# Kernel tuning notes

Hardware: AMD Instinct MI355X
Metric: run time of the kernel (lower is better)

## Reference

```python
import jax, jax.numpy as jnp
import numpy as np

# Module dims (match init_kwargs)
D_IN = 1024
N_PRI = 2048
D_PRI = 16
N_CLS = 25
D_CLS = 16
ITERS = 3
B = 64
EPS = 1e-6


def layer_norm(x, g, b, eps=1e-5):
    m = x.mean(-1, keepdims=True)
    v = ((x - m) ** 2).mean(-1, keepdims=True)
    return (x - m) / jnp.sqrt(v + eps) * g + b


def setup_inputs() -> dict:
    key = jax.random.key(0)
    ks = jax.random.split(key, 6)
    s = lambda n: 1.0 / np.sqrt(n)
    return {
        "z": jax.random.normal(ks[0], (B, D_IN), jnp.float32),
        # to_primary: Linear(d_in, n_primary*d_primary)
        "w1": jax.random.normal(ks[1], (D_IN, N_PRI * D_PRI), jnp.float32) * s(D_IN),
        "b1": jnp.zeros((N_PRI * D_PRI,), jnp.float32),
        # primary_act: LayerNorm(d_in) -> Linear(d_in, n_primary) -> Sigmoid
        "ln1_g": jnp.ones((D_IN,), jnp.float32),
        "ln1_b": jnp.zeros((D_IN,), jnp.float32),
        "w2": jax.random.normal(ks[2], (D_IN, N_PRI), jnp.float32) * s(D_IN),
        "b2": jnp.zeros((N_PRI,), jnp.float32),
        # CapsuleFC transform + EM routing params
        "w_caps": jax.random.normal(ks[3], (N_PRI, D_PRI, N_CLS, D_CLS), jnp.float32) * s(D_PRI),
        "beta_u": jnp.zeros((N_CLS,), jnp.float32),
        "beta_a": jnp.zeros((N_CLS,), jnp.float32),
        # to_logits: LayerNorm(d_class) -> Linear(d_class, 1)
        "ln2_g": jnp.ones((D_CLS,), jnp.float32),
        "ln2_b": jnp.zeros((D_CLS,), jnp.float32),
        "w3": jax.random.normal(ks[4], (D_CLS, 1), jnp.float32) * s(D_CLS),
        "b3": jnp.zeros((1,), jnp.float32),
    }


def em_routing(V, a_in, beta_u, beta_a, n_iter):
    # V: (b, n_in, n_out, d) votes; a_in: (b, n_in) primary activations
    b, n, o, d = V.shape
    R = jnp.full((b, n, o), 1.0 / o, V.dtype)  # routing assignments
    lam = jnp.asarray(1.0, V.dtype)            # inverse temperature
    for _ in range(n_iter):
        # M-step: weighted mean/variance per output capsule
        r = R * a_in[:, :, None]                                  # (b,n,o)
        r_sum = r.sum(axis=1) + EPS                               # (b,o)
        mu = jnp.einsum('bno,bnod->bod', r, V) / r_sum[..., None]  # (b,o,d)
        diff2 = (V - mu[:, None]) ** 2                            # (b,n,o,d)
        sigma2 = jnp.einsum('bno,bnod->bod', r, diff2) / r_sum[..., None] + EPS
        cost = (beta_u[None, :, None] + 0.5 * jnp.log(sigma2)) * r_sum[..., None]
        a_out = jax.nn.sigmoid(lam * (beta_a[None, :] - cost.sum(-1)))  # (b,o)
        # E-step: Gaussian log-likelihood of each vote under each output capsule
        logp = (-0.5 * (diff2 / sigma2[:, None]).sum(-1)
                - 0.5 * jnp.log(sigma2).sum(-1)[:, None, :])      # (b,n,o)
        R = jax.nn.softmax(jnp.log(a_out + EPS)[:, None, :] + logp, axis=-1)
    return mu, a_out, R


def reference(z, w1, b1, ln1_g, ln1_b, w2, b2, w_caps, beta_u, beta_a,
              ln2_g, ln2_b, w3, b3):
    b = z.shape[0]
    # primary poses (no squash: use_squash_primary=False)
    primary_pose = (z @ w1 + b1).reshape(b, N_PRI, D_PRI)
    # primary activations
    primary_act = jnp.clip(jax.nn.sigmoid(layer_norm(z, ln1_g, ln1_b) @ w2 + b2), 0.0, 1.0)
    # votes: each primary capsule predicts each class capsule's pose
    V = jnp.einsum('bni,niod->bnod', primary_pose, w_caps)  # (B, N_PRI, N_CLS, D_CLS)
    class_pose, class_act, q = em_routing(V, primary_act, beta_u, beta_a, ITERS)
    logits = (layer_norm(class_pose, ln2_g, ln2_b) @ w3 + b3).squeeze(-1)  # (B, N_CLS)
    acts = jnp.linalg.norm(class_pose, axis=-1)                            # (B, N_CLS)
    return logits, acts, class_pose, q
```

## Files before the change

### kernel.cpp

```cpp
#include <hip/hip_runtime.h>
#include <hip/hip_bf16.h>
#include <cstdio>

#define B     64
#define DIN   1024
#define NPRI  2048
#define DPRI  16
#define NCLS  25
#define DCLS  16
#define EMEPS 1e-6f
#define LNEPS 1e-5f
#define KS2   8
#define NCHUNK_S 16

#define OFF_POSE 0
#define OFF_ZN   (OFF_POSE + NPRI*DPRI*B)
#define OFF_ACTT (OFF_ZN + B*DIN)
#define OFF_G2P  (OFF_ACTT + NPRI*B)
#define OFF_V    (OFF_G2P + KS2*NPRI*B)
#define V_FLOATS (NPRI*NCLS*B*DCLS/2)
#define OFF_R    (OFF_V + V_FLOATS)
#define R_FLOATS (NPRI*NCLS*B/2)
#define OFF_PART (OFF_R + R_FLOATS)
#define OFF_STAT (OFF_PART + NCLS*NCHUNK_S*33*B)
#define OFF_MU   (OFF_STAT + NCLS*33*B)
#define OFF_MI4  (OFF_MU + NCLS*DCLS*B)
#define OFF_BASE (OFF_MI4 + NCLS*8*B*4)
#define OFF_ZH   (OFF_BASE + NCLS*B)
#define WS_FLOATS (OFF_ZH + B*DIN/2)

typedef __attribute__((ext_vector_type(8))) _Float16 f16x8;
typedef __attribute__((ext_vector_type(4))) float f32x4;

__device__ __forceinline__ unsigned pack_f16(float a, float b) {
  union { _Float16 h[2]; unsigned u; } x;
  x.h[0] = (_Float16)a; x.h[1] = (_Float16)b;
  return x.u;
}
__device__ __forceinline__ float f16lo(unsigned u) {
  union { unsigned u; _Float16 h[2]; } x; x.u = u; return (float)x.h[0];
}
__device__ __forceinline__ float f16hi(unsigned u) {
  union { unsigned u; _Float16 h[2]; } x; x.u = u; return (float)x.h[1];
}
__device__ __forceinline__ unsigned short f16bits(float a) {
  union { _Float16 h; unsigned short u; } x; x.h = (_Float16)a; return x.u;
}
__device__ __forceinline__ float f16val(unsigned short u) {
  union { unsigned short u; _Float16 h; } x; x.u = u; return (float)x.h;
}

__global__ __launch_bounds__(256) void k_zh(const float* __restrict__ z,
                                            unsigned* __restrict__ zh) {
  int idx = blockIdx.x * 256 + threadIdx.x;
  float2 v = ((const float2*)z)[idx];
  zh[idx] = pack_f16(v.x, v.y);
}

__global__ __launch_bounds__(256) void k_ln(const float* __restrict__ z,
                                            const float* __restrict__ g,
                                            const float* __restrict__ bb,
                                            float* __restrict__ zn) {
  int row = blockIdx.x, t = threadIdx.x;
  const float* zr = z + row * DIN;
  float4 v = ((const float4*)zr)[t];
  float s  = v.x + v.y + v.z + v.w;
  float s2 = v.x*v.x + v.y*v.y + v.z*v.z + v.w*v.w;
  for (int off = 32; off; off >>= 1) {
    s  += __shfl_down(s, off);
    s2 += __shfl_down(s2, off);
  }
  __shared__ float ls[8];
  int wv = t >> 6, ln = t & 63;
  if (ln == 0) { ls[wv*2] = s; ls[wv*2+1] = s2; }
  __syncthreads();
  s  = ls[0] + ls[2] + ls[4] + ls[6];
  s2 = ls[1] + ls[3] + ls[5] + ls[7];
  float mean = s * (1.0f / DIN);
  float var  = s2 * (1.0f / DIN) - mean * mean;
  float inv  = 1.0f / sqrtf(var + LNEPS);
  float4 gg = ((const float4*)g)[t];
  float4 bv = ((const float4*)bb)[t];
  float4 o;
  o.x = (v.x - mean) * inv * gg.x + bv.x;
  o.y = (v.y - mean) * inv * gg.y + bv.y;
  o.z = (v.z - mean) * inv * gg.z + bv.z;
  o.w = (v.w - mean) * inv * gg.w + bv.w;
  ((float4*)(zn + row * DIN))[t] = o;
}

__global__ __launch_bounds__(512) void k_gemm1m(const unsigned* __restrict__ zh,
                                                const float* __restrict__ w1,
                                                const float* __restrict__ b1,
                                                float* __restrict__ poseT) {
  __shared__ __align__(16) unsigned bt[2][64 * 68];
  __shared__ __align__(16) unsigned zl[2][64 * 68];
  int t = threadIdx.x;
  int c0 = blockIdx.x * 64;
  int l = t & 63, w = t >> 6;
  int kh = w >> 2, cw = w & 3;
  int c15 = l & 15, kq = l >> 4;
  int h  = t >> 8;
  int th = t & 255;
  int s_kp = th >> 2;
  int s_q  = th & 3;

  f32x4 acc0 = {0,0,0,0}, acc1 = {0,0,0,0}, acc2 = {0,0,0,0}, acc3 = {0,0,0,0};

  for (int it = 0; it < 4; ++it) {
    int k0 = (h * 4 + it) * 128;
#pragma unroll
    for (int u = 0; u < 4; ++u) {
      int cq = s_q + 4 * u;
      const float* src0 = w1 + (size_t)(k0 + 2 * s_kp) * 32768 + c0 + cq * 4;
      float4 r0 = *(const float4*)src0;
      float4 r1 = *(const float4*)(src0 + 32768);
      unsigned* dst = &bt[h][(cq * 4) * 68 + s_kp];
      dst[0]   = pack_f16(r0.x, r1.x);
      dst[68]  = pack_f16(r0.y, r1.y);
      dst[136] = pack_f16(r0.z, r1.z);
      dst[204] = pack_f16(r0.w, r1.w);
    }
#pragma unroll
    for (int u = 0; u < 4; ++u) {
      int ku4 = s_q + 4 * u;
      uint4 v = *(const uint4*)&zh[(size_t)s_kp * 512 + (k0 >> 1) + ku4 * 4];
      *(uint4*)&zl[h][s_kp * 68 + ku4 * 4] = v;
    }
    __syncthreads();
#pragma unroll
    for (int ks = 0; ks < 4; ++ks) {
      union { uint4 u; f16x8 hh; } bf, a0, a1, a2, a3;
      bf.u = *(const uint4*)&bt[kh][(cw * 16 + c15) * 68 + ks * 16 + kq * 4];
      a0.u = *(const uint4*)&zl[kh][(c15)      * 68 + ks * 16 + kq * 4];
      a1.u = *(const uint4*)&zl[kh][(16 + c15) * 68 + ks * 16 + kq * 4];
      a2.u = *(const uint4*)&zl[kh][(32 + c15) * 68 + ks * 16 + kq * 4];
      a3.u = *(const uint4*)&zl[kh][(48 + c15) * 68 + ks * 16 + kq * 4];
      acc0 = __builtin_amdgcn_mfma_f32_16x16x32_f16(a0.hh, bf.hh, acc0, 0, 0, 0);
      acc1 = __builtin_amdgcn_mfma_f32_16x16x32_f16(a1.hh, bf.hh, acc1, 0, 0, 0);
      acc2 = __builtin_amdgcn_mfma_f32_16x16x32_f16(a2.hh, bf.hh, acc2, 0, 0, 0);
      acc3 = __builtin_amdgcn_mfma_f32_16x16x32_f16(a3.hh, bf.hh, acc3, 0, 0, 0);
    }
    __syncthreads();
  }

  float* red = (float*)&zl[0][0];
  if (kh == 1) {
    int cc = cw * 16 + c15;
    *(float4*)&red[cc * 68 + kq * 4]      = *(float4*)&acc0;
    *(float4*)&red[cc * 68 + 16 + kq * 4] = *(float4*)&acc1;
    *(float4*)&red[cc * 68 + 32 + kq * 4] = *(float4*)&acc2;
    *(float4*)&red[cc * 68 + 48 + kq * 4] = *(float4*)&acc3;
  }
  __syncthreads();
  if (kh == 0) {
    int cc = cw * 16 + c15;
    int c = c0 + cc;
    float bc = b1[c];
    float4 r0 = *(float4*)&red[cc * 68 + kq * 4];
    float4 r1 = *(float4*)&red[cc * 68 + 16 + kq * 4];
    float4 r2 = *(float4*)&red[cc * 68 + 32 + kq * 4];
    float4 r3 = *(float4*)&red[cc * 68 + 48 + kq * 4];
    float* pdst = poseT + (size_t)c * 64 + kq * 4;
    float4 o0 = {acc0[0] + r0.x + bc, acc0[1] + r0.y + bc, acc0[2] + r0.z + bc, acc0[3] + r0.w + bc};
    float4 o1 = {acc1[0] + r1.x + bc, acc1[1] + r1.y + bc, acc1[2] + r1.z + bc, acc1[3] + r1.w + bc};
    float4 o2 = {acc2[0] + r2.x + bc, acc2[1] + r2.y + bc, acc2[2] + r2.z + bc, acc2[3] + r2.w + bc};
    float4 o3 = {acc3[0] + r3.x + bc, acc3[1] + r3.y + bc, acc3[2] + r3.z + bc, acc3[3] + r3.w + bc};
    *(float4*)&pdst[0]  = o0;
    *(float4*)&pdst[16] = o1;
    *(float4*)&pdst[32] = o2;
    *(float4*)&pdst[48] = o3;
  }
}

__global__ __launch_bounds__(256, 2) void k_gemm2p(const float* __restrict__ zn,
                                                   const float* __restrict__ w2,
                                                   float* __restrict__ part) {
  __shared__ __align__(16) float znT[128 * 68];
  __shared__ __align__(16) float wl[128 * 68];
  int t = threadIdx.x;
  int c0 = blockIdx.x * 64;
  int k0 = blockIdx.y * 128;
  int zr_ = t >> 2, za = t & 3;
  int wk = t >> 1, wc = (t & 1) * 32;

#pragma unroll
  for (int jj = 0; jj < 4; ++jj) {
    int kb = za * 8 + jj * 32;
    const float* src = zn + zr_ * DIN + k0 + kb;
    float4 v0 = *(const float4*)src;
    float4 v1 = *(const float4*)(src + 4);
    znT[(kb+0)*68 + zr_] = v0.x; znT[(kb+1)*68 + zr_] = v0.y;
    znT[(kb+2)*68 + zr_] = v0.z; znT[(kb+3)*68 + zr_] = v0.w;
    znT[(kb+4)*68 + zr_] = v1.x; znT[(kb+5)*68 + zr_] = v1.y;
    znT[(kb+6)*68 + zr_] = v1.z; znT[(kb+7)*68 + zr_] = v1.w;
  }
  const float* wsrc = w2 + (size_t)(k0 + wk) * NPRI + c0 + wc;
#pragma unroll
  for (int j = 0; j < 8; ++j)
    *(float4*)&wl[wk * 68 + wc + j * 4] = *(const float4*)(wsrc + j * 4);
  __syncthreads();

  int r0 = (t >> 4) * 4, c0l = (t & 15) * 4;
  float acc[4][4];
#pragma unroll
  for (int j = 0; j < 4; ++j)
#pragma unroll
    for (int i = 0; i < 4; ++i) acc[j][i] = 0.f;

#pragma unroll 4
  for (int k = 0; k < 128; ++k) {
    float4 z4 = *(const float4*)&znT[k * 68 + r0];
    float4 w4 = *(const float4*)&wl[k * 68 + c0l];
    float zz[4] = {z4.x, z4.y, z4.z, z4.w};
    float ww[4] = {w4.x, w4.y, w4.z, w4.w};
#pragma unroll
    for (int j = 0; j < 4; ++j)
#pragma unroll
      for (int i = 0; i < 4; ++i) acc[j][i] += ww[j] * zz[i];
  }
  float* pdst = part + ((size_t)blockIdx.y * NPRI + c0 + c0l) * 64 + r0;
#pragma unroll
  for (int j = 0; j < 4; ++j) {
    float4 o = {acc[j][0], acc[j][1], acc[j][2], acc[j][3]};
    *(float4*)&pdst[j * 64] = o;
  }
}

__global__ __launch_bounds__(256) void k_gemm2r(const float* __restrict__ part,
                                                const float* __restrict__ b2,
                                                float* __restrict__ actt) {
  int idx = blockIdx.x * 256 + threadIdx.x;
  float4 s = {0.f, 0.f, 0.f, 0.f};
#pragma unroll
  for (int kz = 0; kz < KS2; ++kz) {
    float4 v = *(const float4*)&part[(size_t)kz * NPRI * 64 + idx * 4];
    s.x += v.x; s.y += v.y; s.z += v.z; s.w += v.w;
  }
  int c = (idx * 4) >> 6;
  float bc = b2[c];
  float4 o;
  o.x = fminf(fmaxf(1.0f / (1.0f + expf(-(s.x + bc))), 0.0f), 1.0f);
  o.y = fminf(fmaxf(1.0f / (1.0f + expf(-(s.y + bc))), 0.0f), 1.0f);
  o.z = fminf(fmaxf(1.0f / (1.0f + expf(-(s.z + bc))), 0.0f), 1.0f);
  o.w = fminf(fmaxf(1.0f / (1.0f + expf(-(s.w + bc))), 0.0f), 1.0f);
  *(float4*)&actt[idx * 4] = o;
}

__global__ __launch_bounds__(256) void k_votes(const float* __restrict__ poseT,
                                               const float* __restrict__ wcaps,
                                               unsigned* __restrict__ V) {
  __shared__ __align__(16) float wl[6400];
  __shared__ __align__(16) float pl[64 * 16];
  int n = blockIdx.x, t = threadIdx.x;
  const float* wsrc = wcaps + (size_t)n * 6400;
  for (int idx = t * 4; idx < 6400; idx += 1024)
    *(float4*)(wl + idx) = *(const float4*)(wsrc + idx);
  {
    float4 v = *(const float4*)(poseT + n * 1024 + t * 4);
    int i = (t * 4) >> 6, b = (t * 4) & 63;
    pl[(b+0)*16 + i] = v.x; pl[(b+1)*16 + i] = v.y;
    pl[(b+2)*16 + i] = v.z; pl[(b+3)*16 + i] = v.w;
  }
  __syncthreads();
  if (t >= 200) return;
  int o = t / 8, d0 = (t % 8) * 2;
  float w0[16], w1_[16];
#pragma unroll
  for (int i = 0; i < 16; ++i) {
    w0[i]  = wl[(i * 25 + o) * 16 + d0];
    w1_[i] = wl[(i * 25 + o) * 16 + d0 + 1];
  }
  unsigned* vd = V + (((size_t)n * 25 + o) * 64 * 16 + d0) / 2;
  for (int b = 0; b < 64; ++b) {
    const float* pb = &pl[b * 16];
    float a0 = 0.f, a1 = 0.f;
#pragma unroll
    for (int i = 0; i < 16; ++i) {
      float p = pb[i];
      a0 += p * w0[i];
      a1 += p * w1_[i];
    }
    vd[b * 8] = pack_f16(a0, a1);
  }
}

template <bool UNIFORM>
__global__ __launch_bounds__(256) void k_stats(const unsigned* __restrict__ V,
                                               const float* __restrict__ actt,
                                               const unsigned short* __restrict__ Rh,
                                               float* __restrict__ part) {
  int o = blockIdx.y;
  int t = threadIdx.x, b = t & 63, wv = t >> 6;
  float S0 = 0.f, S1[16], S2[16];
#pragma unroll
  for (int d = 0; d < 16; ++d) { S1[d] = 0.f; S2[d] = 0.f; }
  int n0 = blockIdx.x * 128 + wv * 32;
  for (int k = 0; k < 32; ++k) {
    int n = n0 + k;
    float a = actt[n * 64 + b];
    float r = UNIFORM ? a * (1.0f / 25.0f)
                      : f16val(Rh[((size_t)n * 25 + o) * 64 + b]) * a;
    const uint4* vp = (const uint4*)(V + (((size_t)n * 25 + o) * 64 + b) * 8);
    uint4 u0 = vp[0], u1 = vp[1];
    unsigned uu[8] = {u0.x, u0.y, u0.z, u0.w, u1.x, u1.y, u1.z, u1.w};
    S0 += r;
#pragma unroll
    for (int q = 0; q < 8; ++q) {
      float v0 = f16lo(uu[q]), v1 = f16hi(uu[q]);
      float t0 = r * v0, t1 = r * v1;
      S1[2*q]   += t0;          S1[2*q+1] += t1;
      S2[2*q]   += t0 * v0;     S2[2*q+1] += t1 * v1;
    }
  }
  __shared__ float red[4 * 33 * 64];
  red[(wv * 33 + 0) * 64 + b] = S0;
#pragma unroll
  for (int d = 0; d < 16; ++d) {
    red[(wv * 33 + 1 + d) * 64 + b]  = S1[d];
    red[(wv * 33 + 17 + d) * 64 + b] = S2[d];
  }
  __syncthreads();
  if (wv == 0) {
    for (int s = 0; s < 33; ++s) {
      float tot = red[s * 64 + b] + red[(33 + s) * 64 + b] +
                  red[(66 + s) * 64 + b] + red[(99 + s) * 64 + b];
      part[((o * NCHUNK_S + blockIdx.x) * 33 + s) * 64 + b] = tot;
    }
  }
}

__global__ __launch_bounds__(256) void k_reduce(const float* __restrict__ part,
                                                float* __restrict__ stats) {
  int o = blockIdx.x;
  for (int idx = threadIdx.x; idx < 33 * 64; idx += 256) {
    float s = 0.f;
#pragma unroll
    for (int c = 0; c < NCHUNK_S; ++c)
      s += part[(o * NCHUNK_S + c) * 33 * 64 + idx];
    stats[o * 33 * 64 + idx] = s;
  }
}

__global__ __launch_bounds__(64) void k_finish(const float* __restrict__ stats,
                                               const float* __restrict__ beta_u,
                                               const float* __restrict__ beta_a,
                                               float* __restrict__ mu,
                                               float* __restrict__ mi4,
                                               float* __restrict__ basew) {
  int o = blockIdx.x, b = threadIdx.x;
  const float* st = stats + o * 33 * 64;
  float s0 = st[b];
  float rs = s0 + EMEPS;
  float inv_rs = 1.0f / rs;
  float ldet = 0.f;
  float mloc[16], iloc[16];
#pragma unroll
  for (int d = 0; d < 16; ++d) {
    float s1 = st[(1 + d) * 64 + b];
    float s2 = st[(17 + d) * 64 + b];
    float m = s1 * inv_rs;
    float var = (s2 - 2.0f * m * s1 + m * m * s0) * inv_rs;
    float sg = fmaxf(var, 0.0f) + EMEPS;
    mloc[d] = m;
    iloc[d] = 1.0f / sg;
    mu[(o * 16 + d) * 64 + b] = m;
    ldet += logf(sg);
  }
#pragma unroll
  for (int q = 0; q < 8; ++q) {
    float4 v = {mloc[2*q], iloc[2*q], mloc[2*q+1], iloc[2*q+1]};
    *(float4*)&mi4[((o * 8 + q) * 64 + b) * 4] = v;
  }
  float cost = (16.0f * beta_u[o] + 0.5f * ldet) * rs;
  float x = beta_a[o] - cost;
  float a = 1.0f / (1.0f + expf(-x));
  basew[o * 64 + b] = logf(a + EMEPS) - 0.5f * ldet;
}

template <bool FINAL>
__global__ __launch_bounds__(256) void k_estep(const unsigned* __restrict__ V,
                                               const float* __restrict__ mi4,
                                               const float* __restrict__ basew,
                                               unsigned short* __restrict__ Rh,
                                               float* __restrict__ qout) {
  int t = threadIdx.x, b = t & 63, ng = t >> 6;
  int n = blockIdx.x * 4 + ng;
  float l[25];
  float mx = -1e30f;
#pragma unroll
  for (int o = 0; o < 25; ++o) {
    const uint4* vp = (const uint4*)(V + (((size_t)n * 25 + o) * 64 + b) * 8);
    uint4 u0 = vp[0], u1 = vp[1];
    unsigned uu[8] = {u0.x, u0.y, u0.z, u0.w, u1.x, u1.y, u1.z, u1.w};
    float acc = 0.f;
#pragma unroll
    for (int qq = 0; qq < 8; ++qq) {
      float4 mi = *(const float4*)&mi4[((o * 8 + qq) * 64 + b) * 4];
      float d0 = f16lo(uu[qq]) - mi.x;
      float d1 = f16hi(uu[qq]) - mi.z;
      acc += d0 * d0 * mi.y + d1 * d1 * mi.w;
    }
    l[o] = basew[o * 64 + b] - 0.5f * acc;
    mx = fmaxf(mx, l[o]);
  }
  float s = 0.f;
#pragma unroll
  for (int o = 0; o < 25; ++o) { l[o] = expf(l[o] - mx); s += l[o]; }
  float inv = 1.0f / s;
  if (FINAL) {
    float* qp = qout + ((size_t)b * NPRI + n) * 25;
#pragma unroll
    for (int o = 0; o < 25; ++o) qp[o] = l[o] * inv;
  } else {
#pragma unroll
    for (int o = 0; o < 25; ++o)
      Rh[((size_t)n * 25 + o) * 64 + b] = f16bits(l[o] * inv);
  }
}

__global__ __launch_bounds__(64) void k_out(const float* __restrict__ mu,
                                            const float* __restrict__ g2,
                                            const float* __restrict__ bb2,
                                            const float* __restrict__ w3,
                                            const float* __restrict__ b3,
                                            float* __restrict__ out) {
  int o = blockIdx.x, b = threadIdx.x;
  float m[16];
  float s = 0.f;
#pragma unroll
  for (int d = 0; d < 16; ++d) { m[d] = mu[(o * 16 + d) * 64 + b]; s += m[d]; }
  float mean = s * (1.0f / 16.0f);
  float var = 0.f;
#pragma unroll
  for (int d = 0; d < 16; ++d) { float dd = m[d] - mean; var += dd * dd; }
  var *= (1.0f / 16.0f);
  float inv = 1.0f / sqrtf(var + LNEPS);
  float logit = 0.f, nrm = 0.f;
#pragma unroll
  for (int d = 0; d < 16; ++d) {
    float nh = (m[d] - mean) * inv * g2[d] + bb2[d];
    logit += nh * w3[d];
    nrm += m[d] * m[d];
  }
  out[b * 25 + o] = logit + b3[0];
  out[1600 + b * 25 + o] = sqrtf(nrm);
  float* pp = out + 3200 + (b * 25 + o) * 16;
#pragma unroll
  for (int d = 0; d < 16; ++d) pp[d] = m[d];
}

extern "C" void kernel_launch(void* const* d_in, const int* in_sizes, int n_in,
                              void* d_out, int out_size, void* d_ws, size_t ws_size,
                              hipStream_t stream) {
  const float* z      = (const float*)d_in[0];
  const float* w1     = (const float*)d_in[1];
  const float* b1     = (const float*)d_in[2];
  const float* ln1g   = (const float*)d_in[3];
  const float* ln1b   = (const float*)d_in[4];
  const float* w2     = (const float*)d_in[5];
  const float* b2     = (const float*)d_in[6];
  const float* wcaps  = (const float*)d_in[7];
  const float* beta_u = (const float*)d_in[8];
  const float* beta_a = (const float*)d_in[9];
  const float* ln2g   = (const float*)d_in[10];
  const float* ln2b   = (const float*)d_in[11];
  const float* w3     = (const float*)d_in[12];
  const float* b3     = (const float*)d_in[13];

  if (ws_size < (size_t)WS_FLOATS * 4) {
    fprintf(stderr, "kernel_launch: ws too small: %zu < %zu bytes\n",
            ws_size, (size_t)WS_FLOATS * 4);
  }

  float* ws    = (float*)d_ws;
  float* out   = (float*)d_out;
  float* poseT = ws + OFF_POSE;
  float* zn    = ws + OFF_ZN;
  float* actt  = ws + OFF_ACTT;
  float* g2p   = ws + OFF_G2P;
  unsigned* V  = (unsigned*)(ws + OFF_V);
  unsigned short* Rh = (unsigned short*)(ws + OFF_R);
  float* part  = ws + OFF_PART;
  float* st    = ws + OFF_STAT;
  float* muw   = ws + OFF_MU;
  float* mi4   = ws + OFF_MI4;
  float* bse   = ws + OFF_BASE;
  unsigned* zh = (unsigned*)(ws + OFF_ZH);

  k_zh<<<128, 256, 0, stream>>>(z, zh);
  k_ln<<<64, 256, 0, stream>>>(z, ln1g, ln1b, zn);
  k_gemm1m<<<512, 512, 0, stream>>>(zh, w1, b1, poseT);
  k_gemm2p<<<dim3(32, KS2), 256, 0, stream>>>(zn, w2, g2p);
  k_gemm2r<<<128, 256, 0, stream>>>(g2p, b2, actt);
  k_votes<<<2048, 256, 0, stream>>>(poseT, wcaps, V);

  k_stats<true><<<dim3(NCHUNK_S, 25), 256, 0, stream>>>(V, actt, Rh, part);
  k_reduce<<<25, 256, 0, stream>>>(part, st);
  k_finish<<<25, 64, 0, stream>>>(st, beta_u, beta_a, muw, mi4, bse);

  for (int it = 0; it < 2; ++it) {
    k_estep<false><<<512, 256, 0, stream>>>(V, mi4, bse, Rh, nullptr);
    k_stats<false><<<dim3(NCHUNK_S, 25), 256, 0, stream>>>(V, actt, Rh, part);
    k_reduce<<<25, 256, 0, stream>>>(part, st);
    k_finish<<<25, 64, 0, stream>>>(st, beta_u, beta_a, muw, mi4, bse);
  }

  k_estep<true><<<512, 256, 0, stream>>>(V, mi4, bse, nullptr, out + 28800);
  k_out<<<25, 64, 0, stream>>>(muw, ln2g, ln2b, w3, b3, out);
}
```

Baseline: 357.9 us.

## Fuse EM E-step with M-step statistics and merge reduce/finish kernels

Each non-final routing iteration now computes the softmax assignments and accumulates the weighted first and second moments in one kernel, so the f16 routing matrix is no longer written and read back. Each thread handles two dims per vote, and the 25-output distance sum is completed with cross-lane shuffles. The partial-sum reduction and the finish step are merged into one kernel, and the LayerNorm and f16 conversion kernels are merged. This removes a large intermediate round trip and several launches, at the cost of 125 accumulators per thread (register pressure) and a larger partial buffer (128 chunks) to reduce.

Result: slower. 614.7 us (+71.8%).

```diff
diff --git a/kernel.cpp b/kernel.cpp
--- a/kernel.cpp
+++ b/kernel.cpp
@@ -12,6 +12,7 @@
 #define LNEPS 1e-5f
 #define KS2   8
 #define NCHUNK_S 16
+#define NCHP  128
 
 #define OFF_POSE 0
 #define OFF_ZN   (OFF_POSE + NPRI*DPRI*B)
@@ -19,11 +20,8 @@
 #define OFF_G2P  (OFF_ACTT + NPRI*B)
 #define OFF_V    (OFF_G2P + KS2*NPRI*B)
 #define V_FLOATS (NPRI*NCLS*B*DCLS/2)
-#define OFF_R    (OFF_V + V_FLOATS)
-#define R_FLOATS (NPRI*NCLS*B/2)
-#define OFF_PART (OFF_R + R_FLOATS)
-#define OFF_STAT (OFF_PART + NCLS*NCHUNK_S*33*B)
-#define OFF_MU   (OFF_STAT + NCLS*33*B)
+#define OFF_PART (OFF_V + V_FLOATS)
+#define OFF_MU   (OFF_PART + NCLS*NCHP*33*B)
 #define OFF_MI4  (OFF_MU + NCLS*DCLS*B)
 #define OFF_BASE (OFF_MI4 + NCLS*8*B*4)
 #define OFF_ZH   (OFF_BASE + NCLS*B)
@@ -43,27 +41,17 @@
 __device__ __forceinline__ float f16hi(unsigned u) {
   union { unsigned u; _Float16 h[2]; } x; x.u = u; return (float)x.h[1];
 }
-__device__ __forceinline__ unsigned short f16bits(float a) {
-  union { _Float16 h; unsigned short u; } x; x.h = (_Float16)a; return x.u;
-}
-__device__ __forceinline__ float f16val(unsigned short u) {
-  union { unsigned short u; _Float16 h; } x; x.u = u; return (float)x.h;
-}
-
-__global__ __launch_bounds__(256) void k_zh(const float* __restrict__ z,
-                                            unsigned* __restrict__ zh) {
-  int idx = blockIdx.x * 256 + threadIdx.x;
-  float2 v = ((const float2*)z)[idx];
-  zh[idx] = pack_f16(v.x, v.y);
-}
-
-__global__ __launch_bounds__(256) void k_ln(const float* __restrict__ z,
-                                            const float* __restrict__ g,
-                                            const float* __restrict__ bb,
-                                            float* __restrict__ zn) {
+
+__global__ __launch_bounds__(256) void k_lnzh(const float* __restrict__ z,
+                                              const float* __restrict__ g,
+                                              const float* __restrict__ bb,
+                                              float* __restrict__ zn,
+                                              unsigned* __restrict__ zh) {
   int row = blockIdx.x, t = threadIdx.x;
   const float* zr = z + row * DIN;
   float4 v = ((const float4*)zr)[t];
+  uint2 hz = {pack_f16(v.x, v.y), pack_f16(v.z, v.w)};
+  *(uint2*)&zh[row * 512 + t * 2] = hz;
   float s  = v.x + v.y + v.z + v.w;
   float s2 = v.x*v.x + v.y*v.y + v.z*v.z + v.w*v.w;
   for (int off = 32; off; off >>= 1) {
@@ -285,11 +273,9 @@
   }
 }
 
-template <bool UNIFORM>
-__global__ __launch_bounds__(256) void k_stats(const unsigned* __restrict__ V,
-                                               const float* __restrict__ actt,
-                                               const unsigned short* __restrict__ Rh,
-                                               float* __restrict__ part) {
+__global__ __launch_bounds__(256) void k_stats1(const unsigned* __restrict__ V,
+                                                const float* __restrict__ actt,
+                                                float* __restrict__ part) {
   int o = blockIdx.y;
   int t = threadIdx.x, b = t & 63, wv = t >> 6;
   float S0 = 0.f, S1[16], S2[16];
@@ -298,9 +284,7 @@
   int n0 = blockIdx.x * 128 + wv * 32;
   for (int k = 0; k < 32; ++k) {
     int n = n0 + k;
-    float a = actt[n * 64 + b];
-    float r = UNIFORM ? a * (1.0f / 25.0f)
-                      : f16val(Rh[((size_t)n * 25 + o) * 64 + b]) * a;
+    float r = actt[n * 64 + b] * (1.0f / 25.0f);
     const uint4* vp = (const uint4*)(V + (((size_t)n * 25 + o) * 64 + b) * 8);
     uint4 u0 = vp[0], u1 = vp[1];
     unsigned uu[8] = {u0.x, u0.y, u0.z, u0.w, u1.x, u1.y, u1.z, u1.w};
@@ -330,60 +314,142 @@
   }
 }
 
-__global__ __launch_bounds__(256) void k_reduce(const float* __restrict__ part,
-                                                float* __restrict__ stats) {
-  int o = blockIdx.x;
-  for (int idx = threadIdx.x; idx < 33 * 64; idx += 256) {
+__global__ __launch_bounds__(512, 2) void k_emstep(const unsigned* __restrict__ V,
+                                                   const float* __restrict__ actt,
+                                                   const float* __restrict__ mi4,
+                                                   const float* __restrict__ basew,
+                                                   float* __restrict__ part) {
+  __shared__ float comb[25 * 33 * 32];
+  int t = threadIdx.x;
+  int l = t & 63, w = t >> 6;
+  int dp = l >> 3, bl = l & 7;
+  int ns = w >> 2;
+  int b32 = (w & 3) * 8 + bl;
+  int b = blockIdx.y * 32 + b32;
+  int chunk = blockIdx.x;
+  int n0 = chunk * 16 + ns * 8;
+
+  float S0[25], S1a[25], S1b[25], S2a[25], S2b[25];
+#pragma unroll
+  for (int o = 0; o < 25; ++o) { S0[o]=0.f; S1a[o]=0.f; S1b[o]=0.f; S2a[o]=0.f; S2b[o]=0.f; }
+
+  for (int i = 0; i < 8; ++i) {
+    int n = n0 + i;
+    float a = actt[n * 64 + b];
+    unsigned v[25];
+    float ql[25];
+#pragma unroll
+    for (int o = 0; o < 25; ++o)
+      v[o] = V[(((size_t)n * 25 + o) * 64 + b) * 8 + dp];
+#pragma unroll
+    for (int o = 0; o < 25; ++o) {
+      float4 mi = *(const float4*)&mi4[((o * 8 + dp) * 64 + b) * 4];
+      float d0 = f16lo(v[o]) - mi.x;
+      float d1 = f16hi(v[o]) - mi.z;
+      ql[o] = d0 * d0 * mi.y + d1 * d1 * mi.w;
+    }
+#pragma unroll
+    for (int o = 0; o < 25; ++o) {
+      ql[o] += __shfl_xor(ql[o], 8);
+      ql[o] += __shfl_xor(ql[o], 16);
+      ql[o] += __shfl_xor(ql[o], 32);
+    }
+    float mx = -1e30f;
+#pragma unroll
+    for (int o = 0; o < 25; ++o) {
+      ql[o] = basew[o * 64 + b] - 0.5f * ql[o];
+      mx = fmaxf(mx, ql[o]);
+    }
     float s = 0.f;
 #pragma unroll
-    for (int c = 0; c < NCHUNK_S; ++c)
-      s += part[(o * NCHUNK_S + c) * 33 * 64 + idx];
-    stats[o * 33 * 64 + idx] = s;
-  }
-}
-
-__global__ __launch_bounds__(64) void k_finish(const float* __restrict__ stats,
-                                               const float* __restrict__ beta_u,
-                                               const float* __restrict__ beta_a,
-                                               float* __restrict__ mu,
-                                               float* __restrict__ mi4,
-                                               float* __restrict__ basew) {
-  int o = blockIdx.x, b = threadIdx.x;
-  const float* st = stats + o * 33 * 64;
-  float s0 = st[b];
-  float rs = s0 + EMEPS;
-  float inv_rs = 1.0f / rs;
-  float ldet = 0.f;
-  float mloc[16], iloc[16];
-#pragma unroll
-  for (int d = 0; d < 16; ++d) {
-    float s1 = st[(1 + d) * 64 + b];
-    float s2 = st[(17 + d) * 64 + b];
-    float m = s1 * inv_rs;
-    float var = (s2 - 2.0f * m * s1 + m * m * s0) * inv_rs;
-    float sg = fmaxf(var, 0.0f) + EMEPS;
-    mloc[d] = m;
-    iloc[d] = 1.0f / sg;
-    mu[(o * 16 + d) * 64 + b] = m;
-    ldet += logf(sg);
-  }
-#pragma unroll
-  for (int q = 0; q < 8; ++q) {
-    float4 v = {mloc[2*q], iloc[2*q], mloc[2*q+1], iloc[2*q+1]};
-    *(float4*)&mi4[((o * 8 + q) * 64 + b) * 4] = v;
-  }
-  float cost = (16.0f * beta_u[o] + 0.5f * ldet) * rs;
-  float x = beta_a[o] - cost;
-  float a = 1.0f / (1.0f + expf(-x));
-  basew[o * 64 + b] = logf(a + EMEPS) - 0.5f * ldet;
-}
-
-template <bool FINAL>
-__global__ __launch_bounds__(256) void k_estep(const unsigned* __restrict__ V,
-                                               const float* __restrict__ mi4,
-                                               const float* __restrict__ basew,
-                                               unsigned short* __restrict__ Rh,
-                                               float* __restrict__ qout) {
+    for (int o = 0; o < 25; ++o) { ql[o] = expf(ql[o] - mx); s += ql[o]; }
+    float rs = a / s;
+#pragma unroll
+    for (int o = 0; o < 25; ++o) {
+      float r = ql[o] * rs;
+      float v0 = f16lo(v[o]), v1 = f16hi(v[o]);
+      float t0 = r * v0, t1 = r * v1;
+      S0[o] += r;
+      S1a[o] += t0;      S1b[o] += t1;
+      S2a[o] += t0 * v0; S2b[o] += t1 * v1;
+    }
+  }
+  if (ns == 1) {
+#pragma unroll
+    for (int o = 0; o < 25; ++o) {
+      if (dp == 0) comb[(o * 33 + 0) * 32 + b32] = S0[o];
+      comb[(o * 33 + 1 + 2*dp) * 32 + b32]  = S1a[o];
+      comb[(o * 33 + 2 + 2*dp) * 32 + b32]  = S1b[o];
+      comb[(o * 33 + 17 + 2*dp) * 32 + b32] = S2a[o];
+      comb[(o * 33 + 18 + 2*dp) * 32 + b32] = S2b[o];
+    }
+  }
+  __syncthreads();
+  if (ns == 0) {
+#pragma unroll
+    for (int o = 0; o < 25; ++o) {
+      float* pp = part + ((size_t)(o * NCHP + chunk) * 33) * 64;
+      if (dp == 0)
+        pp[0 * 64 + b] = S0[o] + comb[(o * 33 + 0) * 32 + b32];
+      pp[(1 + 2*dp) * 64 + b]  = S1a[o] + comb[(o * 33 + 1 + 2*dp) * 32 + b32];
+      pp[(2 + 2*dp) * 64 + b]  = S1b[o] + comb[(o * 33 + 2 + 2*dp) * 32 + b32];
+      pp[(17 + 2*dp) * 64 + b] = S2a[o] + comb[(o * 33 + 17 + 2*dp) * 32 + b32];
+      pp[(18 + 2*dp) * 64 + b] = S2b[o] + comb[(o * 33 + 18 + 2*dp) * 32 + b32];
+    }
+  }
+}
+
+template <int CH>
+__global__ __launch_bounds__(256) void k_redfin(const float* __restrict__ part,
+                                                const float* __restrict__ beta_u,
+                                                const float* __restrict__ beta_a,
+                                                float* __restrict__ mu,
+                                                float* __restrict__ mi4,
+                                                float* __restrict__ basew) {
+  __shared__ float st[33 * 64];
+  int o = blockIdx.x, t = threadIdx.x;
+  for (int slot = t; slot < 33 * 64; slot += 256) {
+    float s = 0.f;
+    const float* pp = part + (size_t)o * CH * 2112 + slot;
+    for (int c = 0; c < CH; ++c) s += pp[(size_t)c * 2112];
+    st[slot] = s;
+  }
+  __syncthreads();
+  if (t < 64) {
+    int b = t;
+    float s0 = st[b];
+    float rsm = s0 + EMEPS;
+    float inv_rs = 1.0f / rsm;
+    float ldet = 0.f;
+    float mloc[16], iloc[16];
+#pragma unroll
+    for (int d = 0; d < 16; ++d) {
+      float s1 = st[(1 + d) * 64 + b];
+      float s2 = st[(17 + d) * 64 + b];
+      float m = s1 * inv_rs;
+      float var = (s2 - 2.0f * m * s1 + m * m * s0) * inv_rs;
+      float sg = fmaxf(var, 0.0f) + EMEPS;
+      mloc[d] = m;
+      iloc[d] = 1.0f / sg;
+      mu[(o * 16 + d) * 64 + b] = m;
+      ldet += logf(sg);
+    }
+#pragma unroll
+    for (int q = 0; q < 8; ++q) {
+      float4 v = {mloc[2*q], iloc[2*q], mloc[2*q+1], iloc[2*q+1]};
+      *(float4*)&mi4[((o * 8 + q) * 64 + b) * 4] = v;
+    }
+    float cost = (16.0f * beta_u[o] + 0.5f * ldet) * rsm;
+    float x = beta_a[o] - cost;
+    float a = 1.0f / (1.0f + expf(-x));
+    basew[o * 64 + b] = logf(a + EMEPS) - 0.5f * ldet;
+  }
+}
+
+__global__ __launch_bounds__(256) void k_estepq(const unsigned* __restrict__ V,
+                                                const float* __restrict__ mi4,
+                                                const float* __restrict__ basew,
+                                                float* __restrict__ qout) {
   int t = threadIdx.x, b = t & 63, ng = t >> 6;
   int n = blockIdx.x * 4 + ng;
   float l[25];
@@ -408,15 +474,9 @@
 #pragma unroll
   for (int o = 0; o < 25; ++o) { l[o] = expf(l[o] - mx); s += l[o]; }
   float inv = 1.0f / s;
-  if (FINAL) {
-    float* qp = qout + ((size_t)b * NPRI + n) * 25;
-#pragma unroll
-    for (int o = 0; o < 25; ++o) qp[o] = l[o] * inv;
-  } else {
-#pragma unroll
-    for (int o = 0; o < 25; ++o)
-      Rh[((size_t)n * 25 + o) * 64 + b] = f16bits(l[o] * inv);
-  }
+  float* qp = qout + ((size_t)b * NPRI + n) * 25;
+#pragma unroll
+  for (int o = 0; o < 25; ++o) qp[o] = l[o] * inv;
 }
 
 __global__ __launch_bounds__(64) void k_out(const float* __restrict__ mu,
@@ -480,32 +540,26 @@
   float* actt  = ws + OFF_ACTT;
   float* g2p   = ws + OFF_G2P;
   unsigned* V  = (unsigned*)(ws + OFF_V);
-  unsigned short* Rh = (unsigned short*)(ws + OFF_R);
   float* part  = ws + OFF_PART;
-  float* st    = ws + OFF_STAT;
   float* muw   = ws + OFF_MU;
   float* mi4   = ws + OFF_MI4;
   float* bse   = ws + OFF_BASE;
   unsigned* zh = (unsigned*)(ws + OFF_ZH);
 
-  k_zh<<<128, 256, 0, stream>>>(z, zh);
-  k_ln<<<64, 256, 0, stream>>>(z, ln1g, ln1b, zn);
+  k_lnzh<<<64, 256, 0, stream>>>(z, ln1g, ln1b, zn, zh);
   k_gemm1m<<<512, 512, 0, stream>>>(zh, w1, b1, poseT);
   k_gemm2p<<<dim3(32, KS2), 256, 0, stream>>>(zn, w2, g2p);
   k_gemm2r<<<128, 256, 0, stream>>>(g2p, b2, actt);
   k_votes<<<2048, 256, 0, stream>>>(poseT, wcaps, V);
 
-  k_stats<true><<<dim3(NCHUNK_S, 25), 256, 0, stream>>>(V, actt, Rh, part);
-  k_reduce<<<25, 256, 0, stream>>>(part, st);
-  k_finish<<<25, 64, 0, stream>>>(st, beta_u, beta_a, muw, mi4, bse);
+  k_stats1<<<dim3(NCHUNK_S, 25), 256, 0, stream>>>(V, actt, part);
+  k_redfin<NCHUNK_S><<<25, 256, 0, stream>>>(part, beta_u, beta_a, muw, mi4, bse);
 
   for (int it = 0; it < 2; ++it) {
-    k_estep<false><<<512, 256, 0, stream>>>(V, mi4, bse, Rh, nullptr);
-    k_stats<false><<<dim3(NCHUNK_S, 25), 256, 0, stream>>>(V, actt, Rh, part);
-    k_reduce<<<25, 256, 0, stream>>>(part, st);
-    k_finish<<<25, 64, 0, stream>>>(st, beta_u, beta_a, muw, mi4, bse);
-  }
-
-  k_estep<true><<<512, 256, 0, stream>>>(V, mi4, bse, nullptr, out + 28800);
+    k_emstep<<<dim3(NCHP, 2), 512, 0, stream>>>(V, actt, mi4, bse, part);
+    k_redfin<NCHP><<<25, 256, 0, stream>>>(part, beta_u, beta_a, muw, mi4, bse);
+  }
+
+  k_estepq<<<512, 256, 0, stream>>>(V, mi4, bse, out + 28800);
   k_out<<<25, 64, 0, stream>>>(muw, ln2g, ln2b, w3, b3, out);
 }
```
